# Kernel optimization log

Hardware: AMD Instinct MI355X
Metric: run time of the kernel (lower is better)

## Reference

```python
import jax, jax.numpy as jnp
import numpy as np

NQ = 23          # number of qubits -> statevector dim 2**23
NC = 23          # circuit width used by config_circuit_fun
NUM_BLOCK = 1    # number of repeated blocks


def _config_circuit(nc, nq, num_block):
    # UID 0 = parametrized single-qubit gate, UID 1 = CNOT
    uid_block = [0] * nc + [1] * (nc - 1)
    qid_block = list(range(nc))
    for q in range(nc - 1):
        # qubitID_fun(q0=q, q1=q+1, Nq) = q*(Nq-1) + (q+1-q-1) % Nq = q*(Nq-1)
        qid_block.append(q * (nq - 1))
    return uid_block * num_block, qid_block * num_block


def _u3(theta):
    # General single-qubit gate U = Rz(a) @ Ry(b) @ Rz(c), theta = (a, b, c)
    a = theta[0].astype(jnp.complex64)
    c = theta[2].astype(jnp.complex64)
    cb = jnp.cos(theta[1] * 0.5).astype(jnp.complex64)
    sb = jnp.sin(theta[1] * 0.5).astype(jnp.complex64)
    ea, eA = jnp.exp(-0.5j * a), jnp.exp(0.5j * a)
    ec, eC = jnp.exp(-0.5j * c), jnp.exp(0.5j * c)
    row0 = jnp.stack([ea * cb * ec, -ea * sb * eC])
    row1 = jnp.stack([eA * sb * ec, eA * cb * eC])
    return jnp.stack([row0, row1])  # (2, 2) complex64


def _apply1(U, q, state):
    # apply 2x2 gate U on qubit q of statevector (length 2**NQ)
    st = state.reshape(2 ** q, 2, -1)
    return jnp.einsum('ij,ajb->aib', U, st).reshape(-1)


def _apply2(U4, q0, q1, state):
    # apply 4x4 gate on qubits (q0, q1), q0 < q1
    st = state.reshape(2 ** q0, 2, 2 ** (q1 - q0 - 1), 2, -1)
    Ut = U4.reshape(2, 2, 2, 2)  # (out0, out1, in0, in1)
    return jnp.einsum('ijkl,akblc->aibjc', Ut, st).reshape(-1)


def setup_inputs() -> dict:
    key = jax.random.key(0)
    k1, k2, k3 = jax.random.split(key, 3)
    depth = (2 * NC - 1) * NUM_BLOCK
    param = jax.random.normal(k1, (depth * 3,), dtype=jnp.float32)
    re = jax.random.normal(k2, (2 ** NQ,), dtype=jnp.float32)
    im = jax.random.normal(k3, (2 ** NQ,), dtype=jnp.float32)
    nrm = jnp.sqrt(jnp.sum(re * re + im * im))
    return {"state_re": re / nrm, "state_im": im / nrm, "param": param}


def reference(state_re, state_im, param):
    uids, qids = _config_circuit(NC, NQ, NUM_BLOCK)
    depth = len(uids)
    th = param.reshape(depth, 3)
    cnot = jnp.array([[1, 0, 0, 0],
                      [0, 1, 0, 0],
                      [0, 0, 0, 1],
                      [0, 0, 1, 0]], dtype=jnp.complex64)
    state = (state_re + 1j * state_im).astype(jnp.complex64)
    for i in range(depth):
        if uids[i] == 0:
            state = _apply1(_u3(th[i]), qids[i], state)
        else:
            q0 = qids[i] // (NQ - 1)
            q1 = (qids[i] - q0 * (NQ - 1) + q0 + 1) % NQ
            state = _apply2(cnot, q0, q1, state)
    # return real/imag stacked (schema has no complex dtype)
    return jnp.stack([jnp.real(state), jnp.imag(state)])
```

## Files before the change

kernel.cpp:

```cpp
#include <hip/hip_runtime.h>
#include <math.h>


#define NTOT (1u << 23)

typedef unsigned int u2 __attribute__((ext_vector_type(2)));

struct G8 { float r00,i00,r01,i01,r10,i10,r11,i11; };

__device__ __forceinline__ G8 u3_lane(const float* __restrict__ p, int q) {
    float a = p[3*q+0], b = p[3*q+1], c = p[3*q+2];
    float cb = cosf(b*0.5f), sb = sinf(b*0.5f);
    float ph = (a+c)*0.5f, m = (a-c)*0.5f;
    float cp = cosf(ph), sp = sinf(ph);
    float cm = cosf(m),  sm = sinf(m);
    G8 g;
    g.r00 =  cb*cp; g.i00 = -cb*sp;
    g.r01 = -sb*cm; g.i01 =  sb*sm;
    g.r10 =  sb*cm; g.i10 =  sb*sm;
    g.r11 =  cb*cp; g.i11 =  cb*sp;
    return g;
}

__device__ __forceinline__ float rdl(float v, int q) {
    return __uint_as_float(__builtin_amdgcn_readlane(__float_as_uint(v), q));
}
__device__ __forceinline__ G8 gread(const G8& m, int q) {
    G8 g;
    g.r00=rdl(m.r00,q); g.i00=rdl(m.i00,q);
    g.r01=rdl(m.r01,q); g.i01=rdl(m.i01,q);
    g.r10=rdl(m.r10,q); g.i10=rdl(m.i10,q);
    g.r11=rdl(m.r11,q); g.i11=rdl(m.i11,q);
    return g;
}

__device__ __forceinline__ void bfs(float& x0r, float& x0i, float& x1r, float& x1i, const G8& g) {
    float y0r = g.r00*x0r - g.i00*x0i + g.r01*x1r - g.i01*x1i;
    float y0i = g.r00*x0i + g.i00*x0r + g.r01*x1i + g.i01*x1r;
    float y1r = g.r10*x0r - g.i10*x0i + g.r11*x1r - g.i11*x1i;
    float y1i = g.r10*x0i + g.i10*x0r + g.r11*x1i + g.i11*x1r;
    x0r=y0r; x0i=y0i; x1r=y1r; x1i=y1i;
}
__device__ __forceinline__ void bf4v(float4& ar, float4& ai, float4& br, float4& bi, const G8& g) {
    bfs(ar.x, ai.x, br.x, bi.x, g);
    bfs(ar.y, ai.y, br.y, bi.y, g);
    bfs(ar.z, ai.z, br.z, bi.z, g);
    bfs(ar.w, ai.w, br.w, bi.w, g);
}
__device__ __forceinline__ void bfc0(float4& r, float4& i, const G8& g) {
    bfs(r.x, i.x, r.y, i.y, g); bfs(r.z, i.z, r.w, i.w, g);
}
__device__ __forceinline__ void bfc1(float4& r, float4& i, const G8& g) {
    bfs(r.x, i.x, r.z, i.z, g); bfs(r.y, i.y, r.w, i.w, g);
}
__device__ __forceinline__ void reg_gate0(float4 (&xr)[4], float4 (&xi)[4], const G8& g) {
    bf4v(xr[0],xi[0],xr[1],xi[1],g); bf4v(xr[2],xi[2],xr[3],xi[3],g);
}
__device__ __forceinline__ void reg_gate1(float4 (&xr)[4], float4 (&xi)[4], const G8& g) {
    bf4v(xr[0],xi[0],xr[2],xi[2],g); bf4v(xr[1],xi[1],xr[3],xi[3],g);
}

__device__ __forceinline__ float p_dpp1(float x) {
    return __uint_as_float((unsigned)__builtin_amdgcn_update_dpp(
        0, (int)__float_as_uint(x), 0xB1, 0xF, 0xF, true));
}
__device__ __forceinline__ float p_dpp2(float x) {
    return __uint_as_float((unsigned)__builtin_amdgcn_update_dpp(
        0, (int)__float_as_uint(x), 0x4E, 0xF, 0xF, true));
}
__device__ __forceinline__ float p_x16(float x, int hi) {
#if __has_builtin(__builtin_amdgcn_permlane16_swap)
    u2 r = __builtin_amdgcn_permlane16_swap(__float_as_uint(x), __float_as_uint(x), false, false);
    return __uint_as_float(hi ? r[0] : r[1]);
#else
    (void)hi;
    return __uint_as_float((unsigned)__builtin_amdgcn_ds_swizzle(
        (int)__float_as_uint(x), 0x401F));
#endif
}
__device__ __forceinline__ float p_x32(float x, int hi) {
#if __has_builtin(__builtin_amdgcn_permlane32_swap)
    u2 r = __builtin_amdgcn_permlane32_swap(__float_as_uint(x), __float_as_uint(x), false, false);
    return __uint_as_float(hi ? r[0] : r[1]);
#else
    (void)hi;
    return __shfl_xor(x, 32, 64);
#endif
}

#define MAKE_PGATE(NAME, FETCH)                                                     \
__device__ __forceinline__ void NAME(float4 (&xr)[4], float4 (&xi)[4],              \
                                     const G8& g, int bit, int hi) {                \
    float cor = bit ? g.r11 : g.r00, coi = bit ? g.i11 : g.i00;                     \
    float cpr = bit ? g.r10 : g.r01, cpi = bit ? g.i10 : g.i01;                     \
    (void)hi;                                                                       \
    _Pragma("unroll")                                                               \
    for (int i = 0; i < 4; ++i) {                                                   \
        float4 pr, pi, nr, ni;                                                      \
        pr.x = FETCH(xr[i].x); pr.y = FETCH(xr[i].y);                               \
        pr.z = FETCH(xr[i].z); pr.w = FETCH(xr[i].w);                               \
        pi.x = FETCH(xi[i].x); pi.y = FETCH(xi[i].y);                               \
        pi.z = FETCH(xi[i].z); pi.w = FETCH(xi[i].w);                               \
        nr.x = cor*xr[i].x - coi*xi[i].x + cpr*pr.x - cpi*pi.x;                     \
        ni.x = cor*xi[i].x + coi*xr[i].x + cpr*pi.x + cpi*pr.x;                     \
        nr.y = cor*xr[i].y - coi*xi[i].y + cpr*pr.y - cpi*pi.y;                     \
        ni.y = cor*xi[i].y + coi*xr[i].y + cpr*pi.y + cpi*pr.y;                     \
        nr.z = cor*xr[i].z - coi*xi[i].z + cpr*pr.z - cpi*pi.z;                     \
        ni.z = cor*xi[i].z + coi*xr[i].z + cpr*pi.z + cpi*pr.z;                     \
        nr.w = cor*xr[i].w - coi*xi[i].w + cpr*pr.w - cpi*pi.w;                     \
        ni.w = cor*xi[i].w + coi*xr[i].w + cpr*pi.w + cpi*pr.w;                     \
        xr[i] = nr; xi[i] = ni;                                                     \
    }                                                                               \
}
#define F_DPP1(v) p_dpp1(v)
#define F_DPP2(v) p_dpp2(v)
#define F_X16(v)  p_x16(v, hi)
#define F_X32(v)  p_x32(v, hi)
MAKE_PGATE(gate_dpp1, F_DPP1)
MAKE_PGATE(gate_dpp2, F_DPP2)
MAKE_PGATE(gate_x16,  F_X16)
MAKE_PGATE(gate_x32,  F_X32)

__device__ __forceinline__ int pxor12(int x) { x^=x>>1; x^=x>>2; x^=x>>4; x^=x>>8; return x & 0xFFF; }
__device__ __forceinline__ int pxor9(int x)  { x^=x>>1; x^=x>>2; x^=x>>4; x^=x>>8; return x & 0x1FF; }

__device__ __forceinline__ void highA(float4 (&xr)[4], float4 (&xi)[4],
                                      const G8& my, int h16, int h32) {
    { G8 g = gread(my,22);
#pragma unroll
      for (int j = 0; j < 4; ++j) bfc0(xr[j], xi[j], g); }
    { G8 g = gread(my,21);
#pragma unroll
      for (int j = 0; j < 4; ++j) bfc1(xr[j], xi[j], g); }
    { G8 g = gread(my,5); reg_gate0(xr, xi, g); }
    { G8 g = gread(my,4); reg_gate1(xr, xi, g); }
    { G8 g = gread(my,7); gate_x16(xr, xi, g, h16, h16); }
    { G8 g = gread(my,6); gate_x32(xr, xi, g, h32, h32); }
}
__device__ __forceinline__ void wr_high(char* L, int l, int w,
                                        const float4 (&xr)[4], const float4 (&xi)[4]) {
    const int wslot = ((w << 8) | l) << 4;
#pragma unroll
    for (int j = 0; j < 4; ++j) {
        int a = wslot | (j << 10);
        *(float4*)(L + a) = xr[j];
        *(float4*)(L + a + 65536) = xi[j];
    }
}
__device__ __forceinline__ void rd_high(const char* L, int l, int w,
                                        float4 (&xr)[4], float4 (&xi)[4]) {
    const int sbase = (((l >> 1) & 7) | ((w & 3) << 4) | (((w >> 2) & 3) << 6)
                    | (((l >> 4) & 3) << 9) | ((l & 1) << 11)) << 4;
    constexpr int OFF[4] = {0, 8 << 4, 256 << 4, 264 << 4};
#pragma unroll
    for (int j = 0; j < 4; ++j) {
        int a = sbase | OFF[j];
        xr[j] = *(const float4*)(L + a);
        xi[j] = *(const float4*)(L + a + 65536);
    }
}
__device__ __forceinline__ void highB_store(float4 (&xr)[4], float4 (&xi)[4],
        const G8& my, int l, int w, int blk, int b1, int h16, int h32,
        float4* __restrict__ OR4, float4* __restrict__ OI4) {
    { G8 g = gread(my,8); reg_gate0(xr, xi, g); }
    { G8 g = gread(my,3); reg_gate1(xr, xi, g); }
    { G8 g = gread(my,0); gate_dpp1(xr, xi, g, b1, 0); }
    { G8 g = gread(my,2); gate_x16(xr, xi, g, h16, h16); }
    { G8 g = gread(my,1); gate_x32(xr, xi, g, h32, h32); }
    const int row_base = ((w & 15) << 1) | (((l >> 4) & 3) << 6) | ((l & 1) << 8);
    const int sg = pxor9(row_base);
    const size_t ob = ((size_t)blk << 3) | (size_t)((l >> 1) & 7);
    constexpr int SJ[4] = {0, 0x01, 0x3F, 0x3E};
#pragma unroll
    for (int j = 0; j < 4; ++j) {
        size_t F = (((size_t)(sg ^ SJ[j])) << 12) | ob;
        OR4[F] = xr[j]; OI4[F] = xi[j];
    }
}

__global__ __launch_bounds__(1024, 4)
void pass_high(const float* __restrict__ in_re, const float* __restrict__ in_im,
               const float* __restrict__ param,
               float* __restrict__ out_re, float* __restrict__ out_im) {
    __shared__ __align__(16) char L[131072];
    const int tid = threadIdx.x;
    const int l = tid & 63, w = tid >> 6;
    const int blkA = blockIdx.x, blkB = blockIdx.x + 256;

    const float4* R4p = (const float4*)in_re;
    const float4* I4p = (const float4*)in_im;
    float4 ar[4], ai[4], br_[4], bi_[4];
    const int rb = (l >> 3) | (w << 5);
    const size_t gA = ((size_t)blkA << 3) | (size_t)(l & 7);
    const size_t gB = ((size_t)blkB << 3) | (size_t)(l & 7);
#pragma unroll
    for (int j = 0; j < 4; ++j) {
        size_t gi = (((size_t)(rb | (j << 3))) << 12) | gA;
        ar[j] = R4p[gi]; ai[j] = I4p[gi];
    }
#pragma unroll
    for (int j = 0; j < 4; ++j) {
        size_t gi = (((size_t)(rb | (j << 3))) << 12) | gB;
        br_[j] = R4p[gi]; bi_[j] = I4p[gi];
    }
    G8 my = u3_lane(param, l < 23 ? l : 22);
    const int b1  = l & 1;
    const int h16 = (l >> 4) & 1, h32 = (l >> 5) & 1;
    float4* OR4 = (float4*)out_re;
    float4* OI4 = (float4*)out_im;

    highA(ar, ai, my, h16, h32);
    wr_high(L, l, w, ar, ai);
    __syncthreads();
    rd_high(L, l, w, ar, ai);
    highB_store(ar, ai, my, l, w, blkA, b1, h16, h32, OR4, OI4);
    highA(br_, bi_, my, h16, h32);
    __syncthreads();
    wr_high(L, l, w, br_, bi_);
    __syncthreads();
    rd_high(L, l, w, br_, bi_);
    highB_store(br_, bi_, my, l, w, blkB, b1, h16, h32, OR4, OI4);
}

__device__ __forceinline__ void lowA(float4 (&xr)[4], float4 (&xi)[4],
                                     const G8& my, int b1, int b2, int h16, int h32) {
    { G8 g = gread(my,20); gate_dpp1(xr, xi, g, b1, 0); }
    { G8 g = gread(my,19); gate_dpp2(xr, xi, g, b2, 0); }
    { G8 g = gread(my,16); gate_x16(xr, xi, g, h16, h16); }
    { G8 g = gread(my,15); gate_x32(xr, xi, g, h32, h32); }
    { G8 g = gread(my,14); reg_gate0(xr, xi, g); }
    { G8 g = gread(my,13); reg_gate1(xr, xi, g); }
}
__device__ __forceinline__ void wr_low(char* L, int l, int w,
                                       const float4 (&xr)[4], const float4 (&xi)[4]) {
    const int sw0 = (w << 8) | l;
#pragma unroll
    for (int j = 0; j < 4; ++j) {
        int a = (sw0 | (j << 6)) << 4;
        *(float4*)(L + a) = xr[j];
        *(float4*)(L + a + 65536) = xi[j];
    }
}
__device__ __forceinline__ void rd_low(const char* L, int l, int w,
                                       float4 (&xr)[4], float4 (&xi)[4]) {
    const int sbase = ((l >> 2) & 3) | ((l & 3) << 2) | ((w & 15) << 4)
                    | (((l >> 4) & 3) << 10);
#pragma unroll
    for (int j = 0; j < 4; ++j) {
        int a = (sbase | (j << 8)) << 4;
        xr[j] = *(const float4*)(L + a);
        xi[j] = *(const float4*)(L + a + 65536);
    }
}
__device__ __forceinline__ void lowB_store(float4 (&xr)[4], float4 (&xi)[4],
        const G8& my, int l, int w, int c, int b1, int b2, int h16, int h32,
        float4* __restrict__ R4p, float4* __restrict__ I4p) {
    { G8 g = gread(my,18); gate_dpp1(xr, xi, g, b1, 0); }
    { G8 g = gread(my,17); gate_dpp2(xr, xi, g, b2, 0); }
    { G8 g = gread(my,12); reg_gate0(xr, xi, g); }
    { G8 g = gread(my,11); reg_gate1(xr, xi, g); }
    { G8 g = gread(my,10); gate_x16(xr, xi, g, h16, h16); }
    { G8 g = gread(my, 9); gate_x32(xr, xi, g, h32, h32); }
    const int sbase = ((l >> 2) & 3) | ((l & 3) << 2) | ((w & 15) << 4)
                    | (((l >> 4) & 3) << 10);
    const size_t cb = ((size_t)c) << 12;
    const int px0 = pxor12(sbase);
    const int codd = c & 1;
    const int A12 = codd ? 0xFFF : 0;
    constexpr int PM[4] = {0, 0x1FF, 0x3FF, 0x200};
#pragma unroll
    for (int j = 0; j < 4; ++j) {
        int pxj = px0 ^ PM[j];
        int of4 = pxj ^ A12;
        int b = (pxj ^ codd) & 1;
        float s0r = xr[j].x, s1r = xr[j].y, s2r = xr[j].w, s3r = xr[j].z;
        float s0i = xi[j].x, s1i = xi[j].y, s2i = xi[j].w, s3i = xi[j].z;
        float o0r = b ? s3r : s0r, o1r = b ? s2r : s1r, o2r = b ? s1r : s2r, o3r = b ? s0r : s3r;
        float o0i = b ? s3i : s0i, o1i = b ? s2i : s1i, o2i = b ? s1i : s2i, o3i = b ? s0i : s3i;
        size_t oo = cb | (size_t)of4;
        R4p[oo] = make_float4(o0r, o1r, o2r, o3r);
        I4p[oo] = make_float4(o0i, o1i, o2i, o3i);
    }
}

__global__ __launch_bounds__(1024, 4)
void pass_low(float* __restrict__ sre, float* __restrict__ sim,
              const float* __restrict__ param) {
    __shared__ __align__(16) char L[131072];
    const int tid = threadIdx.x;
    const int l = tid & 63, w = tid >> 6;
    const int cA = blockIdx.x, cB = blockIdx.x + 256;

    float4* R4p = (float4*)sre;
    float4* I4p = (float4*)sim;
    float4 ar[4], ai[4], br_[4], bi_[4];
    const int sw0 = (w << 8) | l;
    const size_t cbA = ((size_t)cA) << 12;
    const size_t cbB = ((size_t)cB) << 12;
#pragma unroll
    for (int j = 0; j < 4; ++j) {
        size_t fi = cbA + (size_t)(sw0 | (j << 6));
        ar[j] = R4p[fi]; ai[j] = I4p[fi];
    }
#pragma unroll
    for (int j = 0; j < 4; ++j) {
        size_t fi = cbB + (size_t)(sw0 | (j << 6));
        br_[j] = R4p[fi]; bi_[j] = I4p[fi];
    }
    G8 my = u3_lane(param, l < 23 ? l : 22);
    const int b1 = l & 1, b2 = (l >> 1) & 1;
    const int h16 = (l >> 4) & 1, h32 = (l >> 5) & 1;

    lowA(ar, ai, my, b1, b2, h16, h32);
    wr_low(L, l, w, ar, ai);
    __syncthreads();
    rd_low(L, l, w, ar, ai);
    lowB_store(ar, ai, my, l, w, cA, b1, b2, h16, h32, R4p, I4p);
    lowA(br_, bi_, my, b1, b2, h16, h32);
    __syncthreads();
    wr_low(L, l, w, br_, bi_);
    __syncthreads();
    rd_low(L, l, w, br_, bi_);
    lowB_store(br_, bi_, my, l, w, cB, b1, b2, h16, h32, R4p, I4p);
}

extern "C" void kernel_launch(void* const* d_in, const int* in_sizes, int n_in,
                              void* d_out, int out_size, void* d_ws, size_t ws_size,
                              hipStream_t stream) {
    (void)in_sizes; (void)n_in; (void)d_ws; (void)ws_size; (void)out_size;
    const float* in_re = (const float*)d_in[0];
    const float* in_im = (const float*)d_in[1];
    const float* param = (const float*)d_in[2];
    float* out_re = (float*)d_out;
    float* out_im = (float*)d_out + NTOT;

    pass_high<<<256, 1024, 0, stream>>>(in_re, in_im, param, out_re, out_im);
    pass_low <<<256, 1024, 0, stream>>>(out_re, out_im, param);
}
```

Baseline: 76.22 us.

## Rework low pass to keep 16 float4 per thread and drop LDS transpose

The low-qubit pass now has each thread hold 16 float4 pairs in registers. All ten low gates are applied with DPP, ds_swizzle and permlane cross-lane fetches plus in-register butterflies, which removes the shared-memory write/read round trip and two barriers. Gates 19 and 20 move from the low pass into the high pass. The launch changes to 512 blocks of 256 threads. The cost is much higher register pressure from 128 live floats per thread, and possibly lower occupancy.

Result: slower. 96.01 us (+26.0%).

```diff
diff --git a/kernel.cpp b/kernel.cpp
--- a/kernel.cpp
+++ b/kernel.cpp
@@ -59,6 +59,13 @@
 __device__ __forceinline__ void reg_gate1(float4 (&xr)[4], float4 (&xi)[4], const G8& g) {
     bf4v(xr[0],xi[0],xr[2],xi[2],g); bf4v(xr[1],xi[1],xr[3],xi[3],g);
 }
+template<int K, int N>
+__device__ __forceinline__ void reg_gateK(float4 (&xr)[N], float4 (&xi)[N], const G8& g) {
+#pragma unroll
+    for (int j = 0; j < N; ++j)
+        if (!(j & (1 << K)))
+            bf4v(xr[j], xi[j], xr[j | (1 << K)], xi[j | (1 << K)], g);
+}
 
 __device__ __forceinline__ float p_dpp1(float x) {
     return __uint_as_float((unsigned)__builtin_amdgcn_update_dpp(
@@ -67,6 +74,14 @@
 __device__ __forceinline__ float p_dpp2(float x) {
     return __uint_as_float((unsigned)__builtin_amdgcn_update_dpp(
         0, (int)__float_as_uint(x), 0x4E, 0xF, 0xF, true));
+}
+__device__ __forceinline__ float p_swz4(float x) {
+    return __uint_as_float((unsigned)__builtin_amdgcn_ds_swizzle(
+        (int)__float_as_uint(x), 0x101F));
+}
+__device__ __forceinline__ float p_swz8(float x) {
+    return __uint_as_float((unsigned)__builtin_amdgcn_ds_swizzle(
+        (int)__float_as_uint(x), 0x201F));
 }
 __device__ __forceinline__ float p_x16(float x, int hi) {
 #if __has_builtin(__builtin_amdgcn_permlane16_swap)
@@ -89,13 +104,14 @@
 }
 
 #define MAKE_PGATE(NAME, FETCH)                                                     \
-__device__ __forceinline__ void NAME(float4 (&xr)[4], float4 (&xi)[4],              \
+template<int N>                                                                     \
+__device__ __forceinline__ void NAME(float4 (&xr)[N], float4 (&xi)[N],              \
                                      const G8& g, int bit, int hi) {                \
     float cor = bit ? g.r11 : g.r00, coi = bit ? g.i11 : g.i00;                     \
     float cpr = bit ? g.r10 : g.r01, cpi = bit ? g.i10 : g.i01;                     \
     (void)hi;                                                                       \
     _Pragma("unroll")                                                               \
-    for (int i = 0; i < 4; ++i) {                                                   \
+    for (int i = 0; i < N; ++i) {                                                   \
         float4 pr, pi, nr, ni;                                                      \
         pr.x = FETCH(xr[i].x); pr.y = FETCH(xr[i].y);                               \
         pr.z = FETCH(xr[i].z); pr.w = FETCH(xr[i].w);                               \
@@ -114,10 +130,14 @@
 }
 #define F_DPP1(v) p_dpp1(v)
 #define F_DPP2(v) p_dpp2(v)
+#define F_SWZ4(v) p_swz4(v)
+#define F_SWZ8(v) p_swz8(v)
 #define F_X16(v)  p_x16(v, hi)
 #define F_X32(v)  p_x32(v, hi)
 MAKE_PGATE(gate_dpp1, F_DPP1)
 MAKE_PGATE(gate_dpp2, F_DPP2)
+MAKE_PGATE(gate_swz4, F_SWZ4)
+MAKE_PGATE(gate_swz8, F_SWZ8)
 MAKE_PGATE(gate_x16,  F_X16)
 MAKE_PGATE(gate_x32,  F_X32)
 
@@ -125,13 +145,15 @@
 __device__ __forceinline__ int pxor9(int x)  { x^=x>>1; x^=x>>2; x^=x>>4; x^=x>>8; return x & 0x1FF; }
 
 __device__ __forceinline__ void highA(float4 (&xr)[4], float4 (&xi)[4],
-                                      const G8& my, int h16, int h32) {
+                                      const G8& my, int b1, int b2, int h16, int h32) {
     { G8 g = gread(my,22);
 #pragma unroll
       for (int j = 0; j < 4; ++j) bfc0(xr[j], xi[j], g); }
     { G8 g = gread(my,21);
 #pragma unroll
       for (int j = 0; j < 4; ++j) bfc1(xr[j], xi[j], g); }
+    { G8 g = gread(my,20); gate_dpp1(xr, xi, g, b1, 0); }
+    { G8 g = gread(my,19); gate_dpp2(xr, xi, g, b2, 0); }
     { G8 g = gread(my,5); reg_gate0(xr, xi, g); }
     { G8 g = gread(my,4); reg_gate1(xr, xi, g); }
     { G8 g = gread(my,7); gate_x16(xr, xi, g, h16, h16); }
@@ -204,17 +226,17 @@
         br_[j] = R4p[gi]; bi_[j] = I4p[gi];
     }
     G8 my = u3_lane(param, l < 23 ? l : 22);
-    const int b1  = l & 1;
+    const int b1  = l & 1, b2 = (l >> 1) & 1;
     const int h16 = (l >> 4) & 1, h32 = (l >> 5) & 1;
     float4* OR4 = (float4*)out_re;
     float4* OI4 = (float4*)out_im;
 
-    highA(ar, ai, my, h16, h32);
+    highA(ar, ai, my, b1, b2, h16, h32);
     wr_high(L, l, w, ar, ai);
     __syncthreads();
     rd_high(L, l, w, ar, ai);
     highB_store(ar, ai, my, l, w, blkA, b1, h16, h32, OR4, OI4);
-    highA(br_, bi_, my, h16, h32);
+    highA(br_, bi_, my, b1, b2, h16, h32);
     __syncthreads();
     wr_high(L, l, w, br_, bi_);
     __syncthreads();
@@ -222,55 +244,45 @@
     highB_store(br_, bi_, my, l, w, blkB, b1, h16, h32, OR4, OI4);
 }
 
-__device__ __forceinline__ void lowA(float4 (&xr)[4], float4 (&xi)[4],
-                                     const G8& my, int b1, int b2, int h16, int h32) {
-    { G8 g = gread(my,20); gate_dpp1(xr, xi, g, b1, 0); }
-    { G8 g = gread(my,19); gate_dpp2(xr, xi, g, b2, 0); }
-    { G8 g = gread(my,16); gate_x16(xr, xi, g, h16, h16); }
-    { G8 g = gread(my,15); gate_x32(xr, xi, g, h32, h32); }
-    { G8 g = gread(my,14); reg_gate0(xr, xi, g); }
-    { G8 g = gread(my,13); reg_gate1(xr, xi, g); }
-}
-__device__ __forceinline__ void wr_low(char* L, int l, int w,
-                                       const float4 (&xr)[4], const float4 (&xi)[4]) {
-    const int sw0 = (w << 8) | l;
-#pragma unroll
-    for (int j = 0; j < 4; ++j) {
-        int a = (sw0 | (j << 6)) << 4;
-        *(float4*)(L + a) = xr[j];
-        *(float4*)(L + a + 65536) = xi[j];
-    }
-}
-__device__ __forceinline__ void rd_low(const char* L, int l, int w,
-                                       float4 (&xr)[4], float4 (&xi)[4]) {
-    const int sbase = ((l >> 2) & 3) | ((l & 3) << 2) | ((w & 15) << 4)
-                    | (((l >> 4) & 3) << 10);
-#pragma unroll
-    for (int j = 0; j < 4; ++j) {
-        int a = (sbase | (j << 8)) << 4;
-        xr[j] = *(const float4*)(L + a);
-        xi[j] = *(const float4*)(L + a + 65536);
-    }
-}
-__device__ __forceinline__ void lowB_store(float4 (&xr)[4], float4 (&xi)[4],
-        const G8& my, int l, int w, int c, int b1, int b2, int h16, int h32,
-        float4* __restrict__ R4p, float4* __restrict__ I4p) {
-    { G8 g = gread(my,18); gate_dpp1(xr, xi, g, b1, 0); }
-    { G8 g = gread(my,17); gate_dpp2(xr, xi, g, b2, 0); }
-    { G8 g = gread(my,12); reg_gate0(xr, xi, g); }
-    { G8 g = gread(my,11); reg_gate1(xr, xi, g); }
-    { G8 g = gread(my,10); gate_x16(xr, xi, g, h16, h16); }
-    { G8 g = gread(my, 9); gate_x32(xr, xi, g, h32, h32); }
-    const int sbase = ((l >> 2) & 3) | ((l & 3) << 2) | ((w & 15) << 4)
-                    | (((l >> 4) & 3) << 10);
+__global__ __launch_bounds__(256, 2)
+void pass_low(float* __restrict__ sre, float* __restrict__ sim,
+              const float* __restrict__ param) {
+    const int tid = threadIdx.x, c = blockIdx.x;
+    const int l = tid & 63, w = tid >> 6;
+    G8 my = u3_lane(param, l < 23 ? l : 22);
+    float4 xr[16], xi[16];
+
+    float4* R4p = (float4*)sre;
+    float4* I4p = (float4*)sim;
     const size_t cb = ((size_t)c) << 12;
-    const int px0 = pxor12(sbase);
+    const int base = (l << 2) | w;
+#pragma unroll
+    for (int j = 0; j < 16; ++j) {
+        size_t fi = cb | (size_t)((j << 8) | base);
+        xr[j] = R4p[fi]; xi[j] = I4p[fi];
+    }
+    asm volatile("s_waitcnt vmcnt(0)" ::: "memory");
+    __syncthreads();
+
+    { G8 g = gread(my,18); gate_dpp1(xr, xi, g, l & 1, 0); }
+    { G8 g = gread(my,17); gate_dpp2(xr, xi, g, (l >> 1) & 1, 0); }
+    { G8 g = gread(my,16); gate_swz4(xr, xi, g, (l >> 2) & 1, 0); }
+    { G8 g = gread(my,15); gate_swz8(xr, xi, g, (l >> 3) & 1, 0); }
+    { G8 g = gread(my,14); gate_x16(xr, xi, g, (l >> 4) & 1, (l >> 4) & 1); }
+    { G8 g = gread(my,13); gate_x32(xr, xi, g, (l >> 5) & 1, (l >> 5) & 1); }
+    { G8 g = gread(my,12); reg_gateK<0>(xr, xi, g); }
+    { G8 g = gread(my,11); reg_gateK<1>(xr, xi, g); }
+    { G8 g = gread(my,10); reg_gateK<2>(xr, xi, g); }
+    { G8 g = gread(my, 9); reg_gateK<3>(xr, xi, g); }
+
+    const int pxb = pxor12(base);
     const int codd = c & 1;
     const int A12 = codd ? 0xFFF : 0;
-    constexpr int PM[4] = {0, 0x1FF, 0x3FF, 0x200};
-#pragma unroll
-    for (int j = 0; j < 4; ++j) {
-        int pxj = px0 ^ PM[j];
+    constexpr int PXJ[16] = {0x000,0x1FF,0x3FF,0x200,0x7FF,0x600,0x400,0x5FF,
+                             0xFFF,0xE00,0xC00,0xDFF,0x800,0x9FF,0xBFF,0xA00};
+#pragma unroll
+    for (int j = 0; j < 16; ++j) {
+        int pxj = pxb ^ PXJ[j];
         int of4 = pxj ^ A12;
         int b = (pxj ^ codd) & 1;
         float s0r = xr[j].x, s1r = xr[j].y, s2r = xr[j].w, s3r = xr[j].z;
@@ -283,47 +295,6 @@
     }
 }
 
-__global__ __launch_bounds__(1024, 4)
-void pass_low(float* __restrict__ sre, float* __restrict__ sim,
-              const float* __restrict__ param) {
-    __shared__ __align__(16) char L[131072];
-    const int tid = threadIdx.x;
-    const int l = tid & 63, w = tid >> 6;
-    const int cA = blockIdx.x, cB = blockIdx.x + 256;
-
-    float4* R4p = (float4*)sre;
-    float4* I4p = (float4*)sim;
-    float4 ar[4], ai[4], br_[4], bi_[4];
-    const int sw0 = (w << 8) | l;
-    const size_t cbA = ((size_t)cA) << 12;
-    const size_t cbB = ((size_t)cB) << 12;
-#pragma unroll
-    for (int j = 0; j < 4; ++j) {
-        size_t fi = cbA + (size_t)(sw0 | (j << 6));
-        ar[j] = R4p[fi]; ai[j] = I4p[fi];
-    }
-#pragma unroll
-    for (int j = 0; j < 4; ++j) {
-        size_t fi = cbB + (size_t)(sw0 | (j << 6));
-        br_[j] = R4p[fi]; bi_[j] = I4p[fi];
-    }
-    G8 my = u3_lane(param, l < 23 ? l : 22);
-    const int b1 = l & 1, b2 = (l >> 1) & 1;
-    const int h16 = (l >> 4) & 1, h32 = (l >> 5) & 1;
-
-    lowA(ar, ai, my, b1, b2, h16, h32);
-    wr_low(L, l, w, ar, ai);
-    __syncthreads();
-    rd_low(L, l, w, ar, ai);
-    lowB_store(ar, ai, my, l, w, cA, b1, b2, h16, h32, R4p, I4p);
-    lowA(br_, bi_, my, b1, b2, h16, h32);
-    __syncthreads();
-    wr_low(L, l, w, br_, bi_);
-    __syncthreads();
-    rd_low(L, l, w, br_, bi_);
-    lowB_store(br_, bi_, my, l, w, cB, b1, b2, h16, h32, R4p, I4p);
-}
-
 extern "C" void kernel_launch(void* const* d_in, const int* in_sizes, int n_in,
                               void* d_out, int out_size, void* d_ws, size_t ws_size,
                               hipStream_t stream) {
@@ -335,5 +306,5 @@
     float* out_im = (float*)d_out + NTOT;
 
     pass_high<<<256, 1024, 0, stream>>>(in_re, in_im, param, out_re, out_im);
-    pass_low <<<256, 1024, 0, stream>>>(out_re, out_im, param);
-}
+    pass_low <<<512, 256, 0, stream>>>(out_re, out_im, param);
+}
```
